# Performance work log

Hardware: AMD Instinct MI355X
Metric: run time of the kernel (lower is better)

The kernel has to match this reference:

```python
import jax, jax.numpy as jnp
import numpy as np

EMBED_DIM = 256
N_LEVELS = 4
N_HEADS = 8
N_POINTS = 4
HEAD_DIM = EMBED_DIM // N_HEADS
N_QUERIES = 8192
BATCH = 2
LEVEL_SHAPES = np.array([[128, 128], [64, 64], [32, 32], [16, 16]], dtype=np.int32)
HMAX, WMAX = 128, 128
EPS = 1e-5


def setup_inputs() -> dict:
    key = jax.random.key(0)
    ks = jax.random.split(key, 10)
    scale = 1.0 / np.sqrt(EMBED_DIM)
    query = jax.random.normal(ks[0], (N_QUERIES, EMBED_DIM), jnp.float32)
    xy_reference_points = jax.random.uniform(ks[1], (N_QUERIES, 2), jnp.float32, 0.05, 0.95)
    val = jax.random.normal(ks[2], (BATCH, HMAX, WMAX, N_LEVELS, EMBED_DIM), jnp.float32)
    # zero outside each level's valid support (mimics sparse COO: absent entries read as 0)
    hh = jnp.arange(HMAX)[:, None, None]
    ww = jnp.arange(WMAX)[None, :, None]
    lh = jnp.asarray(LEVEL_SHAPES[:, 0])[None, None, :]
    lw = jnp.asarray(LEVEL_SHAPES[:, 1])[None, None, :]
    mask = ((hh < lh) & (ww < lw)).astype(jnp.float32)
    stacked_value_tensors = val * mask[None, :, :, :, None]
    return {
        "query": query,
        "xy_reference_points": xy_reference_points,
        "stacked_value_tensors": stacked_value_tensors,
        "W_off": (jax.random.normal(ks[3], (EMBED_DIM, N_LEVELS * N_POINTS * N_HEADS * 2)) * scale * 0.1).astype(jnp.float32),
        "b_off": (jax.random.normal(ks[4], (N_LEVELS * N_POINTS * N_HEADS * 2,)) * 0.5).astype(jnp.float32),
        "W_attn": (jax.random.normal(ks[5], (EMBED_DIM, N_LEVELS * N_POINTS * N_HEADS)) * scale).astype(jnp.float32),
        "b_attn": jnp.zeros((N_LEVELS * N_POINTS * N_HEADS,), jnp.float32),
        "W_out": (jax.random.normal(ks[6], (EMBED_DIM, EMBED_DIM)) * scale).astype(jnp.float32),
        "b_out": jnp.zeros((EMBED_DIM,), jnp.float32),
        "batch_offsets": jnp.array([0, N_QUERIES // 2], jnp.int32),
        "spatial_shapes": jnp.asarray(LEVEL_SHAPES, jnp.int32),
    }


def reference(query, xy_reference_points, stacked_value_tensors, W_off, b_off,
              W_attn, b_attn, W_out, b_out, batch_offsets, spatial_shapes):
    Q = query.shape[0]
    # sampling offsets & attention weights (torch Linear with W stored [in,out])
    off = (query @ W_off + b_off).reshape(Q, N_LEVELS, N_POINTS, N_HEADS, 2)
    aw = (query @ W_attn + b_attn).reshape(Q, N_LEVELS * N_POINTS, N_HEADS)
    aw = jax.nn.softmax(aw, axis=1).reshape(Q, N_LEVELS, N_POINTS, N_HEADS)
    # sampling locations: sigmoid(inverse_sigmoid(ref) + offsets), then map (0,1)->(-1,1)
    r = jnp.clip(xy_reference_points, 0.0, 1.0)
    inv = jnp.log(jnp.clip(r, EPS, 1.0) / jnp.clip(1.0 - r, EPS, 1.0))
    loc = jax.nn.sigmoid(inv[:, None, None, None, :] + off) * 2.0 - 1.0  # (Q,L,P,H,2)
    # per-query batch index from batch_offsets (start index per batch element)
    bidx = jnp.searchsorted(batch_offsets, jnp.arange(Q), side="right") - 1  # (Q,)
    b = bidx[:, None, None, None]
    h_sz = spatial_shapes[:, 0].astype(loc.dtype)[None, :, None, None]
    w_sz = spatial_shapes[:, 1].astype(loc.dtype)[None, :, None, None]
    x = ((loc[..., 0] + 1.0) * w_sz - 1.0) / 2.0  # (Q,L,P,H)
    y = ((loc[..., 1] + 1.0) * h_sz - 1.0) / 2.0
    x0 = jnp.floor(x).astype(jnp.int32); x1 = x0 + 1
    y0 = jnp.floor(y).astype(jnp.int32); y1 = y0 + 1
    wcap = (spatial_shapes[:, 1] - 1).astype(jnp.int32)[None, :, None, None]
    hcap = (spatial_shapes[:, 0] - 1).astype(jnp.int32)[None, :, None, None]
    x0 = jnp.clip(x0, 0, wcap); x1 = jnp.clip(x1, 0, wcap)
    y0 = jnp.clip(y0, 0, hcap); y1 = jnp.clip(y1, 0, hcap)
    x0f = x0.astype(x.dtype); x1f = x1.astype(x.dtype)
    y0f = y0.astype(y.dtype); y1f = y1.astype(y.dtype)
    wa = (x1f - x) * (y1f - y)  # pairs with (x0,y0), as in source
    wb = (x1f - x) * (y - y0f)  # (x0,y1)
    wc = (x - x0f) * (y1f - y)  # (x1,y0)
    wd = (x - x0f) * (y - y0f)  # (x1,y1)
    V = stacked_value_tensors.reshape(BATCH, HMAX, WMAX, N_LEVELS, N_HEADS, HEAD_DIM)
    l = jnp.arange(N_LEVELS)[None, :, None, None]
    h = jnp.arange(N_HEADS)[None, None, None, :]
    # NOTE: source indexes (batch, x, y, level, head) -> x indexes the height dim; levels are square
    def g(xi, yi):
        return V[b, xi, yi, l, h]  # (Q,L,P,H,HEAD_DIM)
    sampled = (wa[..., None] * g(x0, y0) + wb[..., None] * g(x0, y1)
               + wc[..., None] * g(x1, y0) + wd[..., None] * g(x1, y1))
    out = jnp.einsum("qlphd,qlph->qhd", sampled, aw).reshape(Q, EMBED_DIM)
    return out @ W_out + b_out
```

## Files before the change

kernel.cpp:

```cpp
#include <hip/hip_runtime.h>
#include <math.h>

#define ED      256
#define NL      4
#define NH      8
#define NP      4
#define HD      32
#define HMAX    128
#define WMAX    128
#define NLP     16
#define NC      128
#define NOFF_AW 384
#define QPB     4
#define BSTRIDE (HMAX*WMAX*NL*ED)
#define XSTRIDE (WMAX*NL*ED)
#define YSTRIDE (NL*ED)

typedef __attribute__((ext_vector_type(8))) short    bf16x8;
typedef __attribute__((ext_vector_type(8))) __fp16   f16x8;
typedef __attribute__((ext_vector_type(4))) float    f32x4;

__device__ __forceinline__ unsigned short f2bf(float x) {
    unsigned int u = __float_as_uint(x);
    u = (u + 0x7fffu + ((u >> 16) & 1u)) >> 16;
    return (unsigned short)u;
}

__global__ __launch_bounds__(256) void msda_wconv_kernel(
    const float* __restrict__ W_off,
    const float* __restrict__ W_attn,
    const float* __restrict__ W_out,
    __fp16*         __restrict__ WcatT,
    unsigned short* __restrict__ WoutT)
{
    const int idx = blockIdx.x * 256 + threadIdx.x;
    const int t2 = NOFF_AW * ED;
    const int t3 = ED * ED;
    if (idx < t2) {
        int c = idx >> 8, e = idx & 255;
        float v = (c < ED) ? W_off[e * ED + c] : W_attn[e * NC + (c - ED)];
        WcatT[idx] = (__fp16)v;
    } else if (idx < t2 + t3) {
        int i = idx - t2;
        int c = i >> 8, e = i & 255;
        WoutT[i] = f2bf(W_out[e * ED + c]);
    }
}

__global__ __launch_bounds__(256) void gemm_f16_kernel(
    const float*  __restrict__ A,
    const __fp16* __restrict__ BT,
    const float* __restrict__ bias0,
    const float* __restrict__ bias1,
    float* __restrict__ C,
    int M, int NTOT, int bias_split)
{
    const int wave = threadIdx.x >> 6;
    const int lane = threadIdx.x & 63;
    const int gw   = blockIdx.x * 4 + wave;
    const int ngroups = NTOT >> 6;
    const int mg = gw / ngroups, ng = gw % ngroups;
    const int m16 = mg * 16, n64 = ng * 64;
    if (m16 >= M) return;

    const int mrow = lane & 15;
    const int quad = lane >> 4;

    const float4* Arow = (const float4*)(A + (size_t)(m16 + mrow) * 256 + quad * 8);
    const f16x8* B0 = (const f16x8*)(BT + (size_t)(n64 +  0 + mrow) * 256 + quad * 8);
    const f16x8* B1 = (const f16x8*)(BT + (size_t)(n64 + 16 + mrow) * 256 + quad * 8);
    const f16x8* B2 = (const f16x8*)(BT + (size_t)(n64 + 32 + mrow) * 256 + quad * 8);
    const f16x8* B3 = (const f16x8*)(BT + (size_t)(n64 + 48 + mrow) * 256 + quad * 8);

    f32x4 acc0 = {0.f,0.f,0.f,0.f}, acc1 = acc0, acc2 = acc0, acc3 = acc0;
    #pragma unroll
    for (int kb = 0; kb < 8; ++kb) {
        float4 a0 = Arow[kb * 8 + 0];
        float4 a1 = Arow[kb * 8 + 1];
        float av[8] = {a0.x, a0.y, a0.z, a0.w, a1.x, a1.y, a1.z, a1.w};
        f16x8 ah, al;
        #pragma unroll
        for (int j = 0; j < 8; ++j) {
            __fp16 h = (__fp16)av[j];
            ah[j] = h;
            al[j] = (__fp16)(av[j] - (float)h);
        }
        f16x8 b0 = B0[kb * 4], b1 = B1[kb * 4], b2 = B2[kb * 4], b3 = B3[kb * 4];
        acc0 = __builtin_amdgcn_mfma_f32_16x16x32_f16(ah, b0, acc0, 0, 0, 0);
        acc1 = __builtin_amdgcn_mfma_f32_16x16x32_f16(ah, b1, acc1, 0, 0, 0);
        acc2 = __builtin_amdgcn_mfma_f32_16x16x32_f16(ah, b2, acc2, 0, 0, 0);
        acc3 = __builtin_amdgcn_mfma_f32_16x16x32_f16(ah, b3, acc3, 0, 0, 0);
        acc0 = __builtin_amdgcn_mfma_f32_16x16x32_f16(al, b0, acc0, 0, 0, 0);
        acc1 = __builtin_amdgcn_mfma_f32_16x16x32_f16(al, b1, acc1, 0, 0, 0);
        acc2 = __builtin_amdgcn_mfma_f32_16x16x32_f16(al, b2, acc2, 0, 0, 0);
        acc3 = __builtin_amdgcn_mfma_f32_16x16x32_f16(al, b3, acc3, 0, 0, 0);
    }

    const int col = lane & 15;
    f32x4 accs[4] = {acc0, acc1, acc2, acc3};
    #pragma unroll
    for (int i = 0; i < 4; ++i) {
        int n = n64 + i * 16 + col;
        float b = (n < bias_split) ? bias0[n] : bias1[n - bias_split];
        #pragma unroll
        for (int r = 0; r < 4; ++r) {
            int row = m16 + quad * 4 + r;
            C[(size_t)row * NTOT + n] = accs[i][r] + b;
        }
    }
}

__global__ __launch_bounds__(256) void gemm_bf16_kernel(
    const unsigned short* __restrict__ A,
    const unsigned short* __restrict__ BT,
    const float* __restrict__ bias,
    float* __restrict__ C,
    int M, int NTOT)
{
    const int wave = threadIdx.x >> 6;
    const int lane = threadIdx.x & 63;
    const int gw   = blockIdx.x * 4 + wave;
    const int ngroups = NTOT >> 6;
    const int mg = gw / ngroups, ng = gw % ngroups;
    const int m16 = mg * 16, n64 = ng * 64;
    if (m16 >= M) return;

    const int mrow = lane & 15;
    const int quad = lane >> 4;

    const bf16x8* Arow = (const bf16x8*)(A + (size_t)(m16 + mrow) * 256 + quad * 8);
    const bf16x8* B0 = (const bf16x8*)(BT + (size_t)(n64 +  0 + mrow) * 256 + quad * 8);
    const bf16x8* B1 = (const bf16x8*)(BT + (size_t)(n64 + 16 + mrow) * 256 + quad * 8);
    const bf16x8* B2 = (const bf16x8*)(BT + (size_t)(n64 + 32 + mrow) * 256 + quad * 8);
    const bf16x8* B3 = (const bf16x8*)(BT + (size_t)(n64 + 48 + mrow) * 256 + quad * 8);

    f32x4 acc0 = {0.f,0.f,0.f,0.f}, acc1 = acc0, acc2 = acc0, acc3 = acc0;
    #pragma unroll
    for (int kb = 0; kb < 8; ++kb) {
        bf16x8 af = Arow[kb * 4];
        acc0 = __builtin_amdgcn_mfma_f32_16x16x32_bf16(af, B0[kb * 4], acc0, 0, 0, 0);
        acc1 = __builtin_amdgcn_mfma_f32_16x16x32_bf16(af, B1[kb * 4], acc1, 0, 0, 0);
        acc2 = __builtin_amdgcn_mfma_f32_16x16x32_bf16(af, B2[kb * 4], acc2, 0, 0, 0);
        acc3 = __builtin_amdgcn_mfma_f32_16x16x32_bf16(af, B3[kb * 4], acc3, 0, 0, 0);
    }

    const int col = lane & 15;
    f32x4 accs[4] = {acc0, acc1, acc2, acc3};
    #pragma unroll
    for (int i = 0; i < 4; ++i) {
        int n = n64 + i * 16 + col;
        float b = bias[n];
        #pragma unroll
        for (int r = 0; r < 4; ++r) {
            int row = m16 + quad * 4 + r;
            C[(size_t)row * NTOT + n] = accs[i][r] + b;
        }
    }
}

__global__ __launch_bounds__(256) void msda_sample_kernel(
    const float* __restrict__ refp,
    const float* __restrict__ V,
    const float* __restrict__ off_aw,
    const int*   __restrict__ batch_off,
    int n_batch,
    const int*   __restrict__ spatial,
    unsigned short* __restrict__ out_pre,
    int q_total)
{
    __shared__ float  law[QPB][NC];
    __shared__ float2 sminv[QPB][NH];
    __shared__ float2 sref[QPB];
    __shared__ int4   soff[QPB][NC];
    __shared__ float4 swt[QPB][NC];

    const int t  = threadIdx.x;
    const int q0 = blockIdx.x * QPB;

    {
        const int s = t >> 6, c = t & 63;
        const float* row = off_aw + (size_t)(q0 + s) * NOFF_AW + ED;
        law[s][c]      = row[c];
        law[s][c + 64] = row[c + 64];
    }
    __syncthreads();

    if (t < QPB * NH) {
        const int s = t >> 3, h = t & 7;
        float m = -1e30f;
        #pragma unroll
        for (int lp = 0; lp < NLP; ++lp) m = fmaxf(m, law[s][lp * NH + h]);
        float sum = 0.f;
        #pragma unroll
        for (int lp = 0; lp < NLP; ++lp) sum += __expf(law[s][lp * NH + h] - m);
        sminv[s][h] = make_float2(m, 1.f / sum);
    } else if (t < QPB * NH + QPB) {
        const int s = t - QPB * NH;
        const int qid = q0 + s;
        float rx = refp[qid * 2 + 0], ry = refp[qid * 2 + 1];
        rx = fminf(fmaxf(rx, 0.f), 1.f);
        ry = fminf(fmaxf(ry, 0.f), 1.f);
        float ivx = __logf(fmaxf(rx, 1e-5f) / fmaxf(1.f - rx, 1e-5f));
        float ivy = __logf(fmaxf(ry, 1e-5f) / fmaxf(1.f - ry, 1e-5f));
        sref[s] = make_float2(ivx, ivy);
    }
    __syncthreads();

    {
        const int s = t >> 6;
        const int qid = q0 + s;
        int b = 0;
        for (int i = 1; i < n_batch; ++i)
            if (batch_off[i] <= qid) b = i;
        const int bbase = b * BSTRIDE;
        const float2 iv = sref[s];
        const float* offrow = off_aw + (size_t)qid * NOFF_AW;

        #pragma unroll
        for (int half = 0; half < 2; ++half) {
            const int c = (t & 63) + half * 64;
            const int l = c >> 5;
            const int h = c & 7;
            const int hsz = spatial[l * 2 + 0];
            const int wsz = spatial[l * 2 + 1];
            const int wcap = wsz - 1, hcap = hsz - 1;

            const float2 mi = sminv[s][h];
            const float a = __expf(law[s][c] - mi.x) * mi.y;

            const float ox = offrow[c * 2 + 0], oy = offrow[c * 2 + 1];
            float lx = 2.f / (1.f + __expf(-(iv.x + ox))) - 1.f;
            float ly = 2.f / (1.f + __expf(-(iv.y + oy))) - 1.f;
            float x = ((lx + 1.f) * (float)wsz - 1.f) * 0.5f;
            float y = ((ly + 1.f) * (float)hsz - 1.f) * 0.5f;
            int x0 = (int)floorf(x), y0 = (int)floorf(y);
            int x1 = x0 + 1, y1 = y0 + 1;
            x0 = min(max(x0, 0), wcap); x1 = min(max(x1, 0), wcap);
            y0 = min(max(y0, 0), hcap); y1 = min(max(y1, 0), hcap);
            float x0f = (float)x0, x1f = (float)x1;
            float y0f = (float)y0, y1f = (float)y1;

            float4 w;
            w.x = a * (x1f - x) * (y1f - y);
            w.y = a * (x1f - x) * (y - y0f);
            w.z = a * (x - x0f) * (y1f - y);
            w.w = a * (x - x0f) * (y - y0f);
            swt[s][c] = w;
            const int lbase = bbase + l * ED;
            int4 o;
            o.x = lbase + x0 * XSTRIDE + y0 * YSTRIDE;
            o.y = lbase + x0 * XSTRIDE + y1 * YSTRIDE;
            o.z = lbase + x1 * XSTRIDE + y0 * YSTRIDE;
            o.w = lbase + x1 * XSTRIDE + y1 * YSTRIDE;
            soff[s][c] = o;
        }
    }
    __syncthreads();

    {
        const int s    = t >> 6;
        const int lane = t & 63;
        const int h    = lane >> 3;
        const int d4   = (lane & 7) << 2;
        const int inner = h * HD + d4;
        float4 acc = {0.f, 0.f, 0.f, 0.f};
        #pragma unroll 4
        for (int lp = 0; lp < NLP; ++lp) {
            const int c = lp * NH + h;
            int4   o = soff[s][c];
            float4 w = swt[s][c];
            float4 v0 = *(const float4*)&V[o.x + inner];
            float4 v1 = *(const float4*)&V[o.y + inner];
            float4 v2 = *(const float4*)&V[o.z + inner];
            float4 v3 = *(const float4*)&V[o.w + inner];
            acc.x += w.x*v0.x + w.y*v1.x + w.z*v2.x + w.w*v3.x;
            acc.y += w.x*v0.y + w.y*v1.y + w.z*v2.y + w.w*v3.y;
            acc.z += w.x*v0.z + w.y*v1.z + w.z*v2.z + w.w*v3.z;
            acc.w += w.x*v0.w + w.y*v1.w + w.z*v2.w + w.w*v3.w;
        }
        ushort4 o4;
        o4.x = f2bf(acc.x); o4.y = f2bf(acc.y);
        o4.z = f2bf(acc.z); o4.w = f2bf(acc.w);
        *(ushort4*)&out_pre[(size_t)(q0 + s) * ED + inner] = o4;
    }
}

extern "C" void kernel_launch(void* const* d_in, const int* in_sizes, int n_in,
                              void* d_out, int out_size, void* d_ws, size_t ws_size,
                              hipStream_t stream) {
    const float* query  = (const float*)d_in[0];
    const float* refp   = (const float*)d_in[1];
    const float* V      = (const float*)d_in[2];
    const float* W_off  = (const float*)d_in[3];
    const float* b_off  = (const float*)d_in[4];
    const float* W_attn = (const float*)d_in[5];
    const float* b_attn = (const float*)d_in[6];
    const float* W_out  = (const float*)d_in[7];
    const float* b_out  = (const float*)d_in[8];
    const int*   boff   = (const int*)d_in[9];
    const int*   spat   = (const int*)d_in[10];
    const int n_batch   = in_sizes[9];
    const int nq        = in_sizes[0] / ED;
    float* out = (float*)d_out;

    char* ws = (char*)d_ws;
    float*          off_aw  = (float*)ws;
    __fp16*         WcatT   = (__fp16*)(ws + (size_t)nq*NOFF_AW*4);
    unsigned short* WoutT   = (unsigned short*)(WcatT + NOFF_AW*ED);
    unsigned short* out_pre = WoutT + ED*ED;

    {
        int total = NOFF_AW*ED + ED*ED;
        msda_wconv_kernel<<<(total + 255)/256, 256, 0, stream>>>(
            W_off, W_attn, W_out, WcatT, WoutT);
    }
    {
        int waves = (nq/16) * (NOFF_AW/64);
        gemm_f16_kernel<<<(waves + 3)/4, 256, 0, stream>>>(
            query, WcatT, b_off, b_attn, off_aw, nq, NOFF_AW, ED);
    }
    {
        msda_sample_kernel<<<nq/QPB, 256, 0, stream>>>(
            refp, V, off_aw, boff, n_batch, spat, out_pre, nq);
    }
    {
        int waves = (nq/16) * (ED/64);
        gemm_bf16_kernel<<<(waves + 3)/4, 256, 0, stream>>>(
            out_pre, WoutT, b_out, out, nq, ED);
    }
}
```

Measured before the change: 274.8 us.

## Sort queries by spatial bucket for sampling locality; switch output GEMM to fp16

Adds a single-block counting sort that buckets queries by batch and a 16x16 grid of reference-point positions. The sampling kernel then processes queries in that sorted order, with blocks remapped across 8 XCD chunks so that queries sampling nearby value locations share L2 cache. The intermediate output and W_out move from bf16 to fp16 MFMA. The risks are the extra serial one-block sort launch and the scattered writes to out_pre.

```diff
diff --git a/kernel.cpp b/kernel.cpp
--- a/kernel.cpp
+++ b/kernel.cpp
@@ -12,26 +12,75 @@
 #define NC      128
 #define NOFF_AW 384
 #define QPB     4
+#define NBK     1024
 #define BSTRIDE (HMAX*WMAX*NL*ED)
 #define XSTRIDE (WMAX*NL*ED)
 #define YSTRIDE (NL*ED)
 
-typedef __attribute__((ext_vector_type(8))) short    bf16x8;
 typedef __attribute__((ext_vector_type(8))) __fp16   f16x8;
+typedef __attribute__((ext_vector_type(4))) __fp16   f16x4;
 typedef __attribute__((ext_vector_type(4))) float    f32x4;
 
-__device__ __forceinline__ unsigned short f2bf(float x) {
-    unsigned int u = __float_as_uint(x);
-    u = (u + 0x7fffu + ((u >> 16) & 1u)) >> 16;
-    return (unsigned short)u;
+__global__ __launch_bounds__(1024) void msda_sort_kernel(
+    const float* __restrict__ refp,
+    const int*   __restrict__ batch_off,
+    int n_batch,
+    int* __restrict__ bucket_of,
+    int* __restrict__ perm,
+    int nq)
+{
+    __shared__ int cnt[NBK];
+    __shared__ int scan[NBK];
+    const int t = threadIdx.x;
+    cnt[t] = 0;
+    __syncthreads();
+
+    const int iters = (nq + 1023) >> 10;
+    for (int i = 0; i < iters; ++i) {
+        int q = i * 1024 + t;
+        if (q < nq) {
+            int b = 0;
+            for (int j = 1; j < n_batch; ++j)
+                if (batch_off[j] <= q) b = j;
+            b = min(b, 3);
+            float rx = refp[q * 2 + 0], ry = refp[q * 2 + 1];
+            int bx = min(15, max(0, (int)(rx * 16.f)));
+            int by = min(15, max(0, (int)(ry * 16.f)));
+            int bk = (b << 8) | (by << 4) | bx;
+            bucket_of[q] = bk;
+            atomicAdd(&cnt[bk], 1);
+        }
+    }
+    __syncthreads();
+
+    scan[t] = cnt[t];
+    __syncthreads();
+    for (int d = 1; d < NBK; d <<= 1) {
+        int v = scan[t];
+        int u = (t >= d) ? scan[t - d] : 0;
+        __syncthreads();
+        scan[t] = v + u;
+        __syncthreads();
+    }
+    cnt[t] = scan[t] - cnt[t];
+    __syncthreads();
+
+    for (int i = 0; i < iters; ++i) {
+        int q = i * 1024 + t;
+        if (q < nq) {
+            int bk = bucket_of[q];
+            int pos = atomicAdd(&cnt[bk], 1);
+            perm[pos] = q;
+        }
+    }
 }
 
 __global__ __launch_bounds__(256) void msda_wconv_kernel(
     const float* __restrict__ W_off,
     const float* __restrict__ W_attn,
     const float* __restrict__ W_out,
-    __fp16*         __restrict__ WcatT,
-    unsigned short* __restrict__ WoutT)
+    __fp16* __restrict__ WcatT,
+    __fp16* __restrict__ WoutT)
 {
     const int idx = blockIdx.x * 256 + threadIdx.x;
     const int t2 = NOFF_AW * ED;
@@ -43,7 +92,7 @@
     } else if (idx < t2 + t3) {
         int i = idx - t2;
         int c = i >> 8, e = i & 255;
-        WoutT[i] = f2bf(W_out[e * ED + c]);
+        WoutT[i] = (__fp16)W_out[e * ED + c];
     }
 }
 
@@ -110,9 +159,9 @@
     }
 }
 
-__global__ __launch_bounds__(256) void gemm_bf16_kernel(
-    const unsigned short* __restrict__ A,
-    const unsigned short* __restrict__ BT,
+__global__ __launch_bounds__(256) void gemm_ff16_kernel(
+    const __fp16* __restrict__ A,
+    const __fp16* __restrict__ BT,
     const float* __restrict__ bias,
     float* __restrict__ C,
     int M, int NTOT)
@@ -128,20 +177,20 @@
     const int mrow = lane & 15;
     const int quad = lane >> 4;
 
-    const bf16x8* Arow = (const bf16x8*)(A + (size_t)(m16 + mrow) * 256 + quad * 8);
-    const bf16x8* B0 = (const bf16x8*)(BT + (size_t)(n64 +  0 + mrow) * 256 + quad * 8);
-    const bf16x8* B1 = (const bf16x8*)(BT + (size_t)(n64 + 16 + mrow) * 256 + quad * 8);
-    const bf16x8* B2 = (const bf16x8*)(BT + (size_t)(n64 + 32 + mrow) * 256 + quad * 8);
-    const bf16x8* B3 = (const bf16x8*)(BT + (size_t)(n64 + 48 + mrow) * 256 + quad * 8);
+    const f16x8* Arow = (const f16x8*)(A + (size_t)(m16 + mrow) * 256 + quad * 8);
+    const f16x8* B0 = (const f16x8*)(BT + (size_t)(n64 +  0 + mrow) * 256 + quad * 8);
+    const f16x8* B1 = (const f16x8*)(BT + (size_t)(n64 + 16 + mrow) * 256 + quad * 8);
+    const f16x8* B2 = (const f16x8*)(BT + (size_t)(n64 + 32 + mrow) * 256 + quad * 8);
+    const f16x8* B3 = (const f16x8*)(BT + (size_t)(n64 + 48 + mrow) * 256 + quad * 8);
 
     f32x4 acc0 = {0.f,0.f,0.f,0.f}, acc1 = acc0, acc2 = acc0, acc3 = acc0;
     #pragma unroll
     for (int kb = 0; kb < 8; ++kb) {
-        bf16x8 af = Arow[kb * 4];
-        acc0 = __builtin_amdgcn_mfma_f32_16x16x32_bf16(af, B0[kb * 4], acc0, 0, 0, 0);
-        acc1 = __builtin_amdgcn_mfma_f32_16x16x32_bf16(af, B1[kb * 4], acc1, 0, 0, 0);
-        acc2 = __builtin_amdgcn_mfma_f32_16x16x32_bf16(af, B2[kb * 4], acc2, 0, 0, 0);
-        acc3 = __builtin_amdgcn_mfma_f32_16x16x32_bf16(af, B3[kb * 4], acc3, 0, 0, 0);
+        f16x8 af = Arow[kb * 4];
+        acc0 = __builtin_amdgcn_mfma_f32_16x16x32_f16(af, B0[kb * 4], acc0, 0, 0, 0);
+        acc1 = __builtin_amdgcn_mfma_f32_16x16x32_f16(af, B1[kb * 4], acc1, 0, 0, 0);
+        acc2 = __builtin_amdgcn_mfma_f32_16x16x32_f16(af, B2[kb * 4], acc2, 0, 0, 0);
+        acc3 = __builtin_amdgcn_mfma_f32_16x16x32_f16(af, B3[kb * 4], acc3, 0, 0, 0);
     }
 
     const int col = lane & 15;
@@ -162,24 +211,31 @@
     const float* __restrict__ refp,
     const float* __restrict__ V,
     const float* __restrict__ off_aw,
+    const int*   __restrict__ perm,
     const int*   __restrict__ batch_off,
     int n_batch,
     const int*   __restrict__ spatial,
-    unsigned short* __restrict__ out_pre,
+    __fp16* __restrict__ out_pre,
     int q_total)
 {
+    __shared__ int    sqid[QPB];
     __shared__ float  law[QPB][NC];
     __shared__ float2 sminv[QPB][NH];
     __shared__ float2 sref[QPB];
     __shared__ int4   soff[QPB][NC];
     __shared__ float4 swt[QPB][NC];
 
-    const int t  = threadIdx.x;
-    const int q0 = blockIdx.x * QPB;
+    const int t = threadIdx.x;
+    const int chunk = gridDim.x >> 3;
+    const int pblk  = (blockIdx.x & 7) * chunk + (blockIdx.x >> 3);
+    const int q0 = pblk * QPB;
+
+    if (t < QPB) sqid[t] = perm[q0 + t];
+    __syncthreads();
 
     {
         const int s = t >> 6, c = t & 63;
-        const float* row = off_aw + (size_t)(q0 + s) * NOFF_AW + ED;
+        const float* row = off_aw + (size_t)sqid[s] * NOFF_AW + ED;
         law[s][c]      = row[c];
         law[s][c + 64] = row[c + 64];
     }
@@ -196,7 +252,7 @@
         sminv[s][h] = make_float2(m, 1.f / sum);
     } else if (t < QPB * NH + QPB) {
         const int s = t - QPB * NH;
-        const int qid = q0 + s;
+        const int qid = sqid[s];
         float rx = refp[qid * 2 + 0], ry = refp[qid * 2 + 1];
         rx = fminf(fmaxf(rx, 0.f), 1.f);
         ry = fminf(fmaxf(ry, 0.f), 1.f);
@@ -208,7 +264,7 @@
 
     {
         const int s = t >> 6;
-        const int qid = q0 + s;
+        const int qid = sqid[s];
         int b = 0;
         for (int i = 1; i < n_batch; ++i)
             if (batch_off[i] <= qid) b = i;
@@ -278,10 +334,10 @@
             acc.z += w.x*v0.z + w.y*v1.z + w.z*v2.z + w.w*v3.z;
             acc.w += w.x*v0.w + w.y*v1.w + w.z*v2.w + w.w*v3.w;
         }
-        ushort4 o4;
-        o4.x = f2bf(acc.x); o4.y = f2bf(acc.y);
-        o4.z = f2bf(acc.z); o4.w = f2bf(acc.w);
-        *(ushort4*)&out_pre[(size_t)(q0 + s) * ED + inner] = o4;
+        f16x4 o4;
+        o4[0] = (__fp16)acc.x; o4[1] = (__fp16)acc.y;
+        o4[2] = (__fp16)acc.z; o4[3] = (__fp16)acc.w;
+        *(f16x4*)&out_pre[(size_t)sqid[s] * ED + inner] = o4;
     }
 }
 
@@ -304,28 +360,32 @@
     float* out = (float*)d_out;
 
     char* ws = (char*)d_ws;
-    float*          off_aw  = (float*)ws;
-    __fp16*         WcatT   = (__fp16*)(ws + (size_t)nq*NOFF_AW*4);
-    unsigned short* WoutT   = (unsigned short*)(WcatT + NOFF_AW*ED);
-    unsigned short* out_pre = WoutT + ED*ED;
-
-    {
-        int total = NOFF_AW*ED + ED*ED;
-        msda_wconv_kernel<<<(total + 255)/256, 256, 0, stream>>>(
+    float*   off_aw    = (float*)ws;
+    int*     perm      = (int*)(off_aw + (size_t)nq * NOFF_AW);
+    int*     bucket_of = perm + nq;
+    __fp16*  WcatT     = (__fp16*)(bucket_of + nq);
+    __fp16*  WoutT     = WcatT + NOFF_AW * ED;
+    __fp16*  out_pre   = WoutT + ED * ED;
+
+    msda_sort_kernel<<<1, 1024, 0, stream>>>(refp, boff, n_batch,
+                                             bucket_of, perm, nq);
+    {
+        int total = NOFF_AW * ED + ED * ED;
+        msda_wconv_kernel<<<(total + 255) / 256, 256, 0, stream>>>(
             W_off, W_attn, W_out, WcatT, WoutT);
     }
     {
-        int waves = (nq/16) * (NOFF_AW/64);
-        gemm_f16_kernel<<<(waves + 3)/4, 256, 0, stream>>>(
+        int waves = (nq / 16) * (NOFF_AW / 64);
+        gemm_f16_kernel<<<(waves + 3) / 4, 256, 0, stream>>>(
             query, WcatT, b_off, b_attn, off_aw, nq, NOFF_AW, ED);
     }
     {
-        msda_sample_kernel<<<nq/QPB, 256, 0, stream>>>(
-            refp, V, off_aw, boff, n_batch, spat, out_pre, nq);
-    }
-    {
-        int waves = (nq/16) * (ED/64);
-        gemm_bf16_kernel<<<(waves + 3)/4, 256, 0, stream>>>(
+        msda_sample_kernel<<<nq / QPB, 256, 0, stream>>>(
+            refp, V, off_aw, perm, boff, n_batch, spat, out_pre, nq);
+    }
+    {
+        int waves = (nq / 16) * (ED / 64);
+        gemm_ff16_kernel<<<(waves + 3) / 4, 256, 0, stream>>>(
             out_pre, WoutT, b_out, out, nq, ED);
     }
 }
```

Result: no change. 270.3 us (-1.6%).
